# Optimization experiments

Measured on AMD Instinct MI355X. Metric: run time of the kernel, lower is better.

## Reference

```python
import jax, jax.numpy as jnp
import numpy as np

PATCH = 96
STRIDE = PATCH // 2  # 48


def setup_inputs() -> dict:
    key = jax.random.key(0)
    kx = jax.random.fold_in(key, 0)
    x = jax.random.uniform(kx, (8, 4, 1056, 1056), dtype=jnp.float32)
    mu_pristine = jnp.zeros((36,), dtype=jnp.float32)
    cov_pristine = jnp.eye(36, dtype=jnp.float32)
    return {"x": x, "mu_pristine": mu_pristine, "cov_pristine": cov_pristine}


def _extract_patches(x):
    # x: [B, C, H, W] -> overlapping patches [B, C, N, P, P], stride = P//2
    B, C, H, W = x.shape
    nH = (H - PATCH) // STRIDE + 1
    nW = (W - PATCH) // STRIDE + 1
    idx_h = np.arange(nH)[:, None] * STRIDE + np.arange(PATCH)[None, :]  # [nH, P]
    idx_w = np.arange(nW)[:, None] * STRIDE + np.arange(PATCH)[None, :]  # [nW, P]
    p = x[:, :, idx_h, :]            # [B, C, nH, P, W]
    p = p[:, :, :, :, idx_w]         # [B, C, nH, P, nW, P]
    p = p.transpose(0, 1, 2, 4, 3, 5)  # [B, C, nH, nW, P, P]
    return p.reshape(B, C, nH * nW, PATCH, PATCH)


def reference(x, mu_pristine, cov_pristine):
    patches = _extract_patches(x)  # [B, C, N, P, P]
    mu = patches.mean(axis=(-2, -1))                    # [B, C, N]
    var = patches.var(axis=(-2, -1), ddof=1)            # unbiased, matches torch.var
    gx = jnp.diff(patches, axis=-1)                     # [B, C, N, P, P-1]
    gy = jnp.diff(patches, axis=-2)                     # [B, C, N, P-1, P]
    grad_mag = jnp.sqrt((gx * gx).mean(axis=(-2, -1)) + (gy * gy).mean(axis=(-2, -1)))
    # torch concatenates [mu, var, grad_mag] along channel dim per patch, then means over patches
    feats = jnp.concatenate([mu, var, grad_mag], axis=1).mean(axis=-1)  # [B, 3C]
    d = feats.shape[1]
    mu0 = mu_pristine[:d]
    cov_inv = jnp.linalg.inv(cov_pristine[:d, :d])
    diff = feats - mu0[None, :]
    dist = jnp.sqrt(((diff @ cov_inv) * diff).sum(axis=1))  # Mahalanobis distance [B]
    return dist.mean()
```

## Files before the change

### kernel.cpp

```cpp
#include <hip/hip_runtime.h>
#include <math.h>

#define PATCH 96
#define STRIDE 48
#define NH 21
#define NW 21
#define NP (NH * NW)
#define BATCH 8
#define CHAN 4
#define NBC (BATCH * CHAN)
#define IMG_H 1056
#define IMG_W 1056
#define NBAND 22
#define NCHUNK 22
#define NSTAT 6
#define NPIX 9216.0f
#define NGRAD 9120.0f

__global__ __launch_bounds__(576) void band_stats_kernel(
    const float* __restrict__ x, float* __restrict__ pf) {
  __shared__ float acc[NCHUNK * NSTAT];

  const int t = threadIdx.x;
  const int bc = blockIdx.x / NBAND;
  const int band = blockIdx.x - bc * NBAND;
  const int team = (t >= 288) ? 1 : 0;
  const int tt = t - 288 * team;
  const bool active = tt < 264;
  const int tc = active ? tt : 263;
  const int noff = (tc == 263) ? 3 : 4;
  const int r0 = team * 24;

  const float* rowbase = x + (size_t)bc * (IMG_H * IMG_W)
                           + (size_t)(band * STRIDE + r0) * IMG_W
                           + (size_t)(4 * tc);

  float s1 = 0.f, s2 = 0.f, gxi = 0.f, gxb = 0.f, gyi = 0.f, gyb = 0.f;
  const bool bnd_is_gxb = ((tc % 12) == 11);

#define SUMS_GX(A, nxt)                                                  \
  do {                                                                   \
    s1 += (A).x + (A).y + (A).z + (A).w;                                 \
    s2 += (A).x * (A).x + (A).y * (A).y + (A).z * (A).z + (A).w * (A).w; \
    float d1 = (A).y - (A).x, d2 = (A).z - (A).y, d3 = (A).w - (A).z;    \
    float d4 = (nxt) - (A).w;                                            \
    gxi += d1 * d1 + d2 * d2 + d3 * d3;                                  \
    float bd = d4 * d4;                                                  \
    if (bnd_is_gxb) gxb += bd; else gxi += bd;                           \
  } while (0)

  float4 prev;
  {
    const float4 A = *(const float4*)rowbase;
    const float nxt = rowbase[noff];
    SUMS_GX(A, nxt);
    prev = A;
  }
#pragma unroll 4
  for (int r = 1; r < 24; ++r) {
    const float4 A = *(const float4*)(rowbase + (size_t)r * IMG_W);
    const float nxt = rowbase[(size_t)r * IMG_W + noff];
    SUMS_GX(A, nxt);
    const float e0 = A.x - prev.x, e1 = A.y - prev.y,
                e2 = A.z - prev.z, e3 = A.w - prev.w;
    gyi += e0 * e0 + e1 * e1 + e2 * e2 + e3 * e3;
    prev = A;
  }
  if (team == 0 || band != NBAND - 1) {
    const float4 A = *(const float4*)(rowbase + (size_t)24 * IMG_W);
    const float e0 = A.x - prev.x, e1 = A.y - prev.y,
                e2 = A.z - prev.z, e3 = A.w - prev.w;
    const float g = e0 * e0 + e1 * e1 + e2 * e2 + e3 * e3;
    if (team == 0) gyi += g; else gyb += g;
  }
#undef SUMS_GX

  for (int i = t; i < NCHUNK * NSTAT; i += 576) acc[i] = 0.f;
  __syncthreads();
  if (active) {
    const int chunk = tc / 12;
    atomicAdd(&acc[chunk * NSTAT + 0], s1);
    atomicAdd(&acc[chunk * NSTAT + 1], s2);
    atomicAdd(&acc[chunk * NSTAT + 2], gxi);
    atomicAdd(&acc[chunk * NSTAT + 3], gxb);
    atomicAdd(&acc[chunk * NSTAT + 4], gyi);
    atomicAdd(&acc[chunk * NSTAT + 5], gyb);
  }
  __syncthreads();
  float* dst = pf + (size_t)(bc * NBAND + band) * (NCHUNK * NSTAT);
  for (int i = t; i < NCHUNK * NSTAT; i += 576) dst[i] = acc[i];
}

__global__ __launch_bounds__(512) void patch_feats_kernel(
    const float* __restrict__ pf, float* __restrict__ featsG) {
  __shared__ float S[NBAND * NCHUNK * NSTAT];
  __shared__ float wsum[8][3];

  const int bc = blockIdx.x;
  const int t = threadIdx.x;
  const float* src = pf + (size_t)bc * (NBAND * NCHUNK * NSTAT);
  for (int i = t; i < NBAND * NCHUNK * NSTAT; i += 512) S[i] = src[i];
  __syncthreads();

  float fmu = 0.f, fvar = 0.f, fg = 0.f;
  if (t < NP) {
    const int ph = t / NW, pw = t - ph * NW;
#define AT(b, c, s) S[((b) * NCHUNK + (c)) * NSTAT + (s)]
    float S1 = AT(ph, pw, 0) + AT(ph, pw + 1, 0) + AT(ph + 1, pw, 0) + AT(ph + 1, pw + 1, 0);
    float S2 = AT(ph, pw, 1) + AT(ph, pw + 1, 1) + AT(ph + 1, pw, 1) + AT(ph + 1, pw + 1, 1);
    float Gx = AT(ph, pw, 2) + AT(ph, pw, 3) + AT(ph, pw + 1, 2)
             + AT(ph + 1, pw, 2) + AT(ph + 1, pw, 3) + AT(ph + 1, pw + 1, 2);
    float Gy = AT(ph, pw, 4) + AT(ph, pw, 5) + AT(ph + 1, pw, 4)
             + AT(ph, pw + 1, 4) + AT(ph, pw + 1, 5) + AT(ph + 1, pw + 1, 4);
#undef AT
    fmu = S1 / NPIX;
    fvar = (S2 - S1 * S1 / NPIX) / (NPIX - 1.f);
    fg = sqrtf((Gx + Gy) / NGRAD);
  }
#pragma unroll
  for (int off = 32; off > 0; off >>= 1) {
    fmu += __shfl_xor(fmu, off);
    fvar += __shfl_xor(fvar, off);
    fg += __shfl_xor(fg, off);
  }
  const int wave = t >> 6;
  if ((t & 63) == 0) { wsum[wave][0] = fmu; wsum[wave][1] = fvar; wsum[wave][2] = fg; }
  __syncthreads();
  if (t == 0) {
    float m = 0.f, v = 0.f, g = 0.f;
#pragma unroll
    for (int w = 0; w < 8; ++w) { m += wsum[w][0]; v += wsum[w][1]; g += wsum[w][2]; }
    const int b = bc / CHAN, c = bc - b * CHAN;
    featsG[b * 12 + 0 + c] = m / (float)NP;
    featsG[b * 12 + 4 + c] = v / (float)NP;
    featsG[b * 12 + 8 + c] = g / (float)NP;
  }
}

__global__ __launch_bounds__(64) void finalize_kernel(
    const float* __restrict__ featsG, const float* __restrict__ mu0_full,
    const float* __restrict__ cov_full, float* __restrict__ out) {
  __shared__ float feats_s[96];
  __shared__ double inv_s[12][12];
  __shared__ float dist[BATCH];

  const int t = threadIdx.x;
  feats_s[t] = featsG[t];
  if (t < 32) feats_s[64 + t] = featsG[64 + t];

  double M[12];
#pragma unroll
  for (int r = 0; r < 12; ++r) {
    double v = 0.0;
    if (t < 12) v = (double)cov_full[r * 36 + t];
    else if (t < 24) v = (t - 12 == r) ? 1.0 : 0.0;
    M[r] = v;
  }

#pragma unroll
  for (int k = 0; k < 12; ++k) {
    const double piv = __shfl(M[k], k);
    const double ip = 1.0 / piv;
    M[k] *= ip;
#pragma unroll
    for (int r = 0; r < 12; ++r) {
      if (r == k) continue;
      const double f = __shfl(M[r], k);
      M[r] -= f * M[k];
    }
  }

  if (t >= 12 && t < 24) {
    const int j = t - 12;
#pragma unroll
    for (int r = 0; r < 12; ++r) inv_s[r][j] = M[r];
  }
  __syncthreads();

  if (t < BATCH) {
    double acc = 0.0;
    double d[12];
#pragma unroll
    for (int i = 0; i < 12; ++i)
      d[i] = (double)feats_s[t * 12 + i] - (double)mu0_full[i];
#pragma unroll
    for (int i = 0; i < 12; ++i) {
      double row = 0.0;
#pragma unroll
      for (int j = 0; j < 12; ++j) row += inv_s[i][j] * d[j];
      acc += d[i] * row;
    }
    dist[t] = (float)sqrt(acc);
  }
  __syncthreads();
  if (t == 0) {
    float m = 0.f;
#pragma unroll
    for (int b = 0; b < BATCH; ++b) m += dist[b];
    out[0] = m / (float)BATCH;
  }
}

extern "C" void kernel_launch(void* const* d_in, const int* in_sizes, int n_in,
                              void* d_out, int out_size, void* d_ws, size_t ws_size,
                              hipStream_t stream) {
  const float* x   = (const float*)d_in[0];
  const float* mu0 = (const float*)d_in[1];
  const float* cov = (const float*)d_in[2];
  float* out = (float*)d_out;
  float* pf     = (float*)d_ws;
  float* featsG = pf + (size_t)NBC * NBAND * NCHUNK * NSTAT;

  band_stats_kernel<<<NBC * NBAND, 576, 0, stream>>>(x, pf);
  patch_feats_kernel<<<NBC, 512, 0, stream>>>(pf, featsG);
  finalize_kernel<<<1, 64, 0, stream>>>(featsG, mu0, cov, out);
}
```

Baseline: 228.4 us.

## Use one 48-row team per band, wavefront shuffles for x-gradient, nontemporal loads

```diff
diff --git a/kernel.cpp b/kernel.cpp
--- a/kernel.cpp
+++ b/kernel.cpp
@@ -17,78 +17,85 @@
 #define NPIX 9216.0f
 #define NGRAD 9120.0f
 
-__global__ __launch_bounds__(576) void band_stats_kernel(
+typedef float f32x4 __attribute__((ext_vector_type(4)));
+
+__device__ __forceinline__ f32x4 ntload4(const float* p) {
+  return __builtin_nontemporal_load((const f32x4*)p);
+}
+
+__global__ __launch_bounds__(320) void band_stats_kernel(
     const float* __restrict__ x, float* __restrict__ pf) {
   __shared__ float acc[NCHUNK * NSTAT];
 
   const int t = threadIdx.x;
   const int bc = blockIdx.x / NBAND;
   const int band = blockIdx.x - bc * NBAND;
-  const int team = (t >= 288) ? 1 : 0;
-  const int tt = t - 288 * team;
-  const bool active = tt < 264;
-  const int tc = active ? tt : 263;
-  const int noff = (tc == 263) ? 3 : 4;
-  const int r0 = team * 24;
+  const bool active = t < 264;
+  const int tc = active ? t : 263;
+  const int lane = t & 63;
+  const bool lane0 = (lane == 0);
 
   const float* rowbase = x + (size_t)bc * (IMG_H * IMG_W)
-                           + (size_t)(band * STRIDE + r0) * IMG_W
+                           + (size_t)(band * STRIDE) * IMG_W
                            + (size_t)(4 * tc);
 
-  float s1 = 0.f, s2 = 0.f, gxi = 0.f, gxb = 0.f, gyi = 0.f, gyb = 0.f;
-  const bool bnd_is_gxb = ((tc % 12) == 11);
-
-#define SUMS_GX(A, nxt)                                                  \
+  float s1 = 0.f, s2 = 0.f, gxi = 0.f, dla = 0.f, gyi = 0.f, gyb = 0.f;
+
+#define ROW_SUMS(A, sh)                                                  \
   do {                                                                   \
     s1 += (A).x + (A).y + (A).z + (A).w;                                 \
     s2 += (A).x * (A).x + (A).y * (A).y + (A).z * (A).z + (A).w * (A).w; \
     float d1 = (A).y - (A).x, d2 = (A).z - (A).y, d3 = (A).w - (A).z;    \
-    float d4 = (nxt) - (A).w;                                            \
     gxi += d1 * d1 + d2 * d2 + d3 * d3;                                  \
-    float bd = d4 * d4;                                                  \
-    if (bnd_is_gxb) gxb += bd; else gxi += bd;                           \
+    float dl = (A).x - (sh);                                             \
+    dla += dl * dl;                                                      \
   } while (0)
 
-  float4 prev;
+  f32x4 prev;
   {
-    const float4 A = *(const float4*)rowbase;
-    const float nxt = rowbase[noff];
-    SUMS_GX(A, nxt);
+    f32x4 A = ntload4(rowbase);
+    float sh = __shfl_up(A.w, 1);
+    if (lane0) sh = (tc > 0) ? rowbase[-1] : A.x;
+    ROW_SUMS(A, sh);
     prev = A;
   }
-#pragma unroll 4
-  for (int r = 1; r < 24; ++r) {
-    const float4 A = *(const float4*)(rowbase + (size_t)r * IMG_W);
-    const float nxt = rowbase[(size_t)r * IMG_W + noff];
-    SUMS_GX(A, nxt);
-    const float e0 = A.x - prev.x, e1 = A.y - prev.y,
-                e2 = A.z - prev.z, e3 = A.w - prev.w;
+#pragma unroll 6
+  for (int r = 1; r < 48; ++r) {
+    const float* rp = rowbase + (size_t)r * IMG_W;
+    f32x4 A = ntload4(rp);
+    float sh = __shfl_up(A.w, 1);
+    if (lane0) sh = (tc > 0) ? rp[-1] : A.x;
+    ROW_SUMS(A, sh);
+    float e0 = A.x - prev.x, e1 = A.y - prev.y,
+          e2 = A.z - prev.z, e3 = A.w - prev.w;
     gyi += e0 * e0 + e1 * e1 + e2 * e2 + e3 * e3;
     prev = A;
   }
-  if (team == 0 || band != NBAND - 1) {
-    const float4 A = *(const float4*)(rowbase + (size_t)24 * IMG_W);
-    const float e0 = A.x - prev.x, e1 = A.y - prev.y,
-                e2 = A.z - prev.z, e3 = A.w - prev.w;
-    const float g = e0 * e0 + e1 * e1 + e2 * e2 + e3 * e3;
-    if (team == 0) gyi += g; else gyb += g;
-  }
-#undef SUMS_GX
-
-  for (int i = t; i < NCHUNK * NSTAT; i += 576) acc[i] = 0.f;
+  if (band != NBAND - 1) {
+    f32x4 A = ntload4(rowbase + (size_t)48 * IMG_W);
+    float e0 = A.x - prev.x, e1 = A.y - prev.y,
+          e2 = A.z - prev.z, e3 = A.w - prev.w;
+    gyb = e0 * e0 + e1 * e1 + e2 * e2 + e3 * e3;
+  }
+#undef ROW_SUMS
+
+  for (int i = t; i < NCHUNK * NSTAT; i += 320) acc[i] = 0.f;
   __syncthreads();
   if (active) {
-    const int chunk = tc / 12;
-    atomicAdd(&acc[chunk * NSTAT + 0], s1);
-    atomicAdd(&acc[chunk * NSTAT + 1], s2);
-    atomicAdd(&acc[chunk * NSTAT + 2], gxi);
-    atomicAdd(&acc[chunk * NSTAT + 3], gxb);
-    atomicAdd(&acc[chunk * NSTAT + 4], gyi);
-    atomicAdd(&acc[chunk * NSTAT + 5], gyb);
+    const int m = tc / 12;
+    const bool left_is_boundary = ((tc % 12) == 0);
+    float gxi_tot = gxi + (left_is_boundary ? 0.f : dla);
+    atomicAdd(&acc[m * NSTAT + 0], s1);
+    atomicAdd(&acc[m * NSTAT + 1], s2);
+    atomicAdd(&acc[m * NSTAT + 2], gxi_tot);
+    atomicAdd(&acc[m * NSTAT + 4], gyi);
+    atomicAdd(&acc[m * NSTAT + 5], gyb);
+    if (left_is_boundary && tc > 0)
+      atomicAdd(&acc[(m - 1) * NSTAT + 3], dla);
   }
   __syncthreads();
   float* dst = pf + (size_t)(bc * NBAND + band) * (NCHUNK * NSTAT);
-  for (int i = t; i < NCHUNK * NSTAT; i += 576) dst[i] = acc[i];
+  for (int i = t; i < NCHUNK * NSTAT; i += 320) dst[i] = acc[i];
 }
 
 __global__ __launch_bounds__(512) void patch_feats_kernel(
@@ -211,7 +218,7 @@
   float* pf     = (float*)d_ws;
   float* featsG = pf + (size_t)NBC * NBAND * NCHUNK * NSTAT;
 
-  band_stats_kernel<<<NBC * NBAND, 576, 0, stream>>>(x, pf);
+  band_stats_kernel<<<NBC * NBAND, 320, 0, stream>>>(x, pf);
   patch_feats_kernel<<<NBC, 512, 0, stream>>>(pf, featsG);
   finalize_kernel<<<1, 64, 0, stream>>>(featsG, mu0, cov, out);
 }
```

After: 271.6 us. 1.19x slower.
